# Kernel optimization log

Hardware: AMD Instinct MI355X
Metric: run time of the kernel (lower is better)

Reference implementation:

```python
import jax, jax.numpy as jnp
import numpy as np

B, S, D = 2, 4096, 768
H = 12
HD = D // H  # 64
INNER = 4 * D
EPS = 1e-5


def setup_inputs() -> dict:
    key = jax.random.key(0)
    ks = jax.random.split(key, 12)
    sd = 0.02
    # causal additive mask (GPT-2 style): 0 where allowed, -1e9 where masked
    causal = jnp.tril(jnp.ones((S, S), dtype=bool))
    attention_mask = jnp.where(causal, 0.0, -1e9).astype(jnp.float32)[None, None]
    return {
        "hidden_states": jax.random.normal(ks[0], (B, S, D), dtype=jnp.float32),
        "attention_mask": attention_mask,
        "ln1_g": jnp.ones((D,), jnp.float32),
        "ln1_b": jnp.zeros((D,), jnp.float32),
        "w_attn": jax.random.normal(ks[1], (D, 3 * D), jnp.float32) * sd,
        "b_attn": jnp.zeros((3 * D,), jnp.float32),
        "w_cproj": jax.random.normal(ks[2], (D, D), jnp.float32) * sd,
        "b_cproj": jnp.zeros((D,), jnp.float32),
        "ln2_g": jnp.ones((D,), jnp.float32),
        "ln2_b": jnp.zeros((D,), jnp.float32),
        "w_fc": jax.random.normal(ks[3], (D, INNER), jnp.float32) * sd,
        "b_fc": jnp.zeros((INNER,), jnp.float32),
        "w_fc_proj": jax.random.normal(ks[4], (INNER, D), jnp.float32) * sd,
        "b_fc_proj": jnp.zeros((D,), jnp.float32),
    }


def _layernorm(x, g, b):
    mu = jnp.mean(x, axis=-1, keepdims=True)
    var = jnp.mean(jnp.square(x - mu), axis=-1, keepdims=True)
    return (x - mu) * jax.lax.rsqrt(var + EPS) * g + b


def reference(hidden_states, attention_mask, ln1_g, ln1_b, w_attn, b_attn,
              w_cproj, b_cproj, ln2_g, ln2_b, w_fc, b_fc, w_fc_proj, b_fc_proj):
    residual = hidden_states
    x = _layernorm(hidden_states, ln1_g, ln1_b)
    # qkv projection
    qkv = x @ w_attn + b_attn                       # [B,S,3D]
    q, k, v = jnp.split(qkv, 3, axis=-1)
    q = q.reshape(B, S, H, HD).transpose(0, 2, 1, 3)  # [B,H,S,HD]
    k = k.reshape(B, S, H, HD).transpose(0, 2, 1, 3)
    v = v.reshape(B, S, H, HD).transpose(0, 2, 1, 3)
    scale = HD ** -0.5
    scores = jnp.einsum('bhqd,bhkd->bhqk', q, k) * scale + attention_mask
    attn = jax.nn.softmax(scores, axis=-1)
    ctx = jnp.einsum('bhqk,bhkd->bhqd', attn, v)    # [B,H,S,HD]
    ctx = ctx.transpose(0, 2, 1, 3).reshape(B, S, D)
    attn_out = ctx @ w_cproj + b_cproj
    h = attn_out + residual
    residual = h
    y = _layernorm(h, ln2_g, ln2_b)
    y = jax.nn.gelu(y @ w_fc + b_fc, approximate=False)  # nn.GELU default = exact
    y = y @ w_fc_proj + b_fc_proj
    return y + residual
```

## Files before the change

### kernel.cpp

```cpp
#include <hip/hip_runtime.h>
#include <hip/hip_bf16.h>


#define S_     4096
#define D_     768
#define H_     12
#define HD_    64
#define NB_    2
#define M_     (NB_*S_)
#define QKV_   (3*D_)
#define INNER_ 3072

typedef unsigned short u16;
typedef __attribute__((ext_vector_type(4))) float f32x4;
typedef __attribute__((ext_vector_type(8))) short s16x8;

__device__ __forceinline__ float bf2f(u16 h) {
    union { unsigned int u; float f; } c; c.u = ((unsigned int)h) << 16; return c.f;
}
__device__ __forceinline__ u16 f2bf(float f) {
    union { float f; unsigned int u; } c; c.f = f;
    return (u16)((c.u + 0x7fffu + ((c.u >> 16) & 1u)) >> 16);
}
__device__ __forceinline__ void storev(u16* p, float v) { *p = f2bf(v); }
__device__ __forceinline__ void storev(float* p, float v) { *p = v; }

__device__ __forceinline__ float fexp2(float x) {
#if __has_builtin(__builtin_amdgcn_exp2f)
    return __builtin_amdgcn_exp2f(x);
#else
    return __expf(x * 0.69314718056f);
#endif
}
__device__ __forceinline__ unsigned int packbf(float a, float b) {
    union { __hip_bfloat162 h; unsigned int u; } c;
    c.h = __float22bfloat162_rn(float2{a, b});
    return c.u;
}

__device__ __forceinline__ void gload_lds16(const u16* g, u16* l) {
    __builtin_amdgcn_global_load_lds((const __attribute__((address_space(1))) void*)g,
                                     (__attribute__((address_space(3))) void*)l, 16, 0, 0);
}

#define WAITVM(N) asm volatile("s_waitcnt vmcnt(" #N ")" ::: "memory")

template <typename IT, bool PERM>
__global__ __launch_bounds__(256) void transpose_kernel(const IT* __restrict__ in,
                                                        u16* __restrict__ out,
                                                        int ld_in, int ld_out) {
    __shared__ u16 tile[32][33];
    const int c0 = blockIdx.x * 32, r0 = blockIdx.y * 32;
    const int tx = threadIdx.x & 31, ty = threadIdx.x >> 5;
#pragma unroll
    for (int i = 0; i < 32; i += 8) {
        IT v = in[(size_t)(r0 + ty + i) * ld_in + c0 + tx];
        u16 bv;
        if constexpr (sizeof(IT) == 4) bv = f2bf((float)v); else bv = (u16)v;
        tile[ty + i][tx] = bv;
    }
    __syncthreads();
    int oc = r0 + tx;
    if constexpr (PERM) oc = (oc & ~63) | (((oc & 15) << 2) | ((oc >> 4) & 3));
#pragma unroll
    for (int i = 0; i < 32; i += 8)
        out[(size_t)(c0 + ty + i) * ld_out + oc] = tile[tx][ty + i];
}

__global__ __launch_bounds__(256) void ln_row(const float* __restrict__ x, const float* __restrict__ g,
                                              const float* __restrict__ bb, u16* __restrict__ y,
                                              unsigned int* ctr) {
    const int row = blockIdx.x;
    const int tid = threadIdx.x;
    if (ctr && row == 0 && tid == 0) *ctr = 0u;
    const float* xr = x + (size_t)row * D_;
    float v0 = xr[tid], v1 = xr[tid + 256], v2 = xr[tid + 512];
    float s = v0 + v1 + v2, s2 = v0 * v0 + v1 * v1 + v2 * v2;
#pragma unroll
    for (int d = 32; d >= 1; d >>= 1) { s += __shfl_xor(s, d, 64); s2 += __shfl_xor(s2, d, 64); }
    __shared__ float red[8];
    const int wave = tid >> 6, lane = tid & 63;
    if (lane == 0) { red[wave] = s; red[4 + wave] = s2; }
    __syncthreads();
    s = red[0] + red[1] + red[2] + red[3];
    s2 = red[4] + red[5] + red[6] + red[7];
    const float mu = s * (1.0f / D_);
    const float var = s2 * (1.0f / D_) - mu * mu;
    const float rstd = rsqrtf(var + 1e-5f);
    u16* yr = y + (size_t)row * D_;
    yr[tid]       = f2bf((v0 - mu) * rstd * g[tid]       + bb[tid]);
    yr[tid + 256] = f2bf((v1 - mu) * rstd * g[tid + 256] + bb[tid + 256]);
    yr[tid + 512] = f2bf((v2 - mu) * rstd * g[tid + 512] + bb[tid + 512]);
}

template <int EPI>
__global__ __launch_bounds__(512, 2) void gemm256(const u16* __restrict__ A, const u16* __restrict__ Bt,
                                                  const float* __restrict__ bias,
                                                  u16* __restrict__ C, int M, int N, int K, int nbx) {
    __shared__ u16 As[2][256 * 64];
    __shared__ u16 Bs[2][256 * 64];
    const int tid = threadIdx.x;
    const int wave = tid >> 6, lane = tid & 63;
    const int fr = lane & 15, quad = lane >> 4;
    const int wm = wave >> 2, wn = wave & 3;

    const int nwg = (int)gridDim.x;
    const int id = (int)blockIdx.x;
    const int swz = (id & 7) * (nwg >> 3) + (id >> 3);
    const int by = swz / nbx, bx = swz % nbx;
    const int m0 = by << 8, n0 = bx << 8;

    const int rsub = lane >> 3;
    const int schunk = ((lane & 7) ^ rsub) << 3;
    const u16* Ag = A + (size_t)(m0 + wave * 8 + rsub) * K + schunk;
    const u16* Bg = Bt + (size_t)(n0 + wave * 8 + rsub) * K + schunk;
    const int sdst = wave * 512;

    const f32x4 fz = {0.f, 0.f, 0.f, 0.f};
    f32x4 acc[8][4];
#pragma unroll
    for (int i = 0; i < 8; i++)
#pragma unroll
        for (int j = 0; j < 4; j++) acc[i][j] = fz;

    const int nt = K >> 6;

    auto STAGE_E = [&](int t, int b) {
        const int koff = t << 6;
#pragma unroll
        for (int g = 0; g < 4; g++)
            gload_lds16(Bg + (size_t)(g * 64) * K + koff, &Bs[b][g * 4096 + sdst]);
        gload_lds16(Ag + koff,                   &As[b][0 * 4096 + sdst]);
        gload_lds16(Ag + (size_t)128 * K + koff, &As[b][2 * 4096 + sdst]);
    };
    auto STAGE_L = [&](int t, int b) {
        const int koff = t << 6;
        gload_lds16(Ag + (size_t)64 * K + koff,  &As[b][1 * 4096 + sdst]);
        gload_lds16(Ag + (size_t)192 * K + koff, &As[b][3 * 4096 + sdst]);
    };

    STAGE_E(0, 0);
    STAGE_L(0, 0);
    WAITVM(2);

    for (int t = 0; t < nt; t++) {
        const int b = t & 1;
        __syncthreads();
        const u16* ab = As[b];
        const u16* bb = Bs[b];

        s16x8 bf[4][2], af[4][2];
#pragma unroll
        for (int j = 0; j < 4; j++)
#pragma unroll
            for (int kk = 0; kk < 2; kk++) {
                const int r = wn * 64 + j * 16 + fr;
                const int sl = ((kk * 4 + quad) ^ (r & 7)) << 3;
                bf[j][kk] = *(const s16x8*)(bb + r * 64 + sl);
            }
#pragma unroll
        for (int i = 0; i < 4; i++)
#pragma unroll
            for (int kk = 0; kk < 2; kk++) {
                const int r = wm * 128 + i * 16 + fr;
                const int sl = ((kk * 4 + quad) ^ (r & 7)) << 3;
                af[i][kk] = *(const s16x8*)(ab + r * 64 + sl);
            }
        if (t + 1 < nt) STAGE_E(t + 1, b ^ 1);
#pragma unroll
        for (int kk = 0; kk < 2; kk++)
#pragma unroll
            for (int i = 0; i < 4; i++)
#pragma unroll
                for (int j = 0; j < 4; j++)
                    acc[i][j] = __builtin_amdgcn_mfma_f32_16x16x32_bf16(af[i][kk], bf[j][kk], acc[i][j], 0, 0, 0);

        if (t + 1 < nt) { WAITVM(6); } else { WAITVM(0); }
        __syncthreads();

#pragma unroll
        for (int i = 0; i < 4; i++)
#pragma unroll
            for (int kk = 0; kk < 2; kk++) {
                const int r = wm * 128 + 64 + i * 16 + fr;
                const int sl = ((kk * 4 + quad) ^ (r & 7)) << 3;
                af[i][kk] = *(const s16x8*)(ab + r * 64 + sl);
            }
        if (t + 1 < nt) STAGE_L(t + 1, b ^ 1);
#pragma unroll
        for (int kk = 0; kk < 2; kk++)
#pragma unroll
            for (int i = 0; i < 4; i++)
#pragma unroll
                for (int j = 0; j < 4; j++)
                    acc[4 + i][j] = __builtin_amdgcn_mfma_f32_16x16x32_bf16(af[i][kk], bf[j][kk], acc[4 + i][j], 0, 0, 0);

        if (t + 1 < nt) WAITVM(2);
    }

    const int crow0 = m0 + wm * 128 + quad * 4;
    const int ccol0 = n0 + wn * 64 + fr;
#pragma unroll
    for (int j = 0; j < 4; j++) {
        const int col = ccol0 + j * 16;
        const float bv = bias[col];
#pragma unroll
        for (int i = 0; i < 8; i++) {
#pragma unroll
            for (int r = 0; r < 4; r++) {
                const int row = crow0 + i * 16 + r;
                float v = acc[i][j][r] + bv;
                if constexpr (EPI == 1) v = 0.5f * v * (1.0f + erff(v * 0.70710678118654752f));
                C[(size_t)row * N + col] = f2bf(v);
            }
        }
    }
}

template <int EPI, typename OT>
__global__ __launch_bounds__(256) void gemm_bt64(const u16* __restrict__ A, const u16* __restrict__ Bt,
                                                 const float* __restrict__ bias, const float* res,
                                                 OT* C, int M, int N, int K) {
    __shared__ u16 As[3][128 * 32];
    __shared__ u16 Bs[3][64 * 32];
    const int tid = threadIdx.x;
    const int wave = tid >> 6, lane = tid & 63;
    const int m0 = blockIdx.y << 7, n0 = blockIdx.x << 6;
    const int fr = lane & 15, quad = lane >> 4;

    const int srow = wave * 16 + (lane >> 2);
    const int scol = (lane & 3) * 8;
    const u16* ag0 = A + (size_t)(m0 + srow) * K + scol;
    const u16* ag1 = ag0 + (size_t)64 * K;
    const u16* bg0 = Bt + (size_t)(n0 + srow) * K + scol;

    auto STAGE = [&](int k0, int b) {
        gload_lds16(ag0 + k0, &As[b][wave * 512]);
        gload_lds16(ag1 + k0, &As[b][2048 + wave * 512]);
        gload_lds16(bg0 + k0, &Bs[b][wave * 512]);
    };

    const f32x4 fz = {0.f, 0.f, 0.f, 0.f};
    f32x4 acc[2][4];
#pragma unroll
    for (int i = 0; i < 2; i++)
#pragma unroll
        for (int j = 0; j < 4; j++) acc[i][j] = fz;

    const int a_off = (wave * 32 + fr) * 32 + quad * 8;
    const int b_off = fr * 32 + quad * 8;

    const int nsteps = K >> 5;
    STAGE(0, 0);
    if (nsteps > 1) { STAGE(32, 1); WAITVM(3); } else { WAITVM(0); }
    __syncthreads();

    for (int t = 0; t < nsteps; t++) {
        if (t + 2 < nsteps) STAGE((t + 2) << 5, (t + 2) % 3);
        const u16* a_rd = &As[t % 3][a_off];
        const u16* b_rd = &Bs[t % 3][b_off];
        s16x8 af[2], bfr[4];
#pragma unroll
        for (int u = 0; u < 2; u++) af[u] = *(const s16x8*)(a_rd + u * 16 * 32);
#pragma unroll
        for (int u = 0; u < 4; u++) bfr[u] = *(const s16x8*)(b_rd + u * 16 * 32);
#pragma unroll
        for (int mt = 0; mt < 2; mt++)
#pragma unroll
            for (int nt = 0; nt < 4; nt++)
                acc[mt][nt] = __builtin_amdgcn_mfma_f32_16x16x32_bf16(af[mt], bfr[nt], acc[mt][nt], 0, 0, 0);
        if (t + 2 < nsteps) { WAITVM(3); } else { WAITVM(0); }
        __syncthreads();
    }

    const int crow0 = m0 + wave * 32 + quad * 4;
    const int ccol0 = n0 + fr;
#pragma unroll
    for (int nt = 0; nt < 4; nt++) {
        const int col = ccol0 + nt * 16;
        const float bv = bias[col];
#pragma unroll
        for (int mt = 0; mt < 2; mt++) {
#pragma unroll
            for (int r = 0; r < 4; r++) {
                const int row = crow0 + mt * 16 + r;
                float v = acc[mt][nt][r] + bv;
                if constexpr (EPI == 1) v = 0.5f * v * (1.0f + erff(v * 0.70710678118654752f));
                if constexpr (EPI == 2) v += res[(size_t)row * N + col];
                storev(&C[(size_t)row * N + col], v);
            }
        }
    }
}

#define SCALE_  0.1803368801111f
#define PST_    72
#define NITEMS_ (32 * H_ * NB_)
#define NWORK_  512
__global__ __launch_bounds__(256, 2) void flash_attn(const u16* __restrict__ qkv, const u16* __restrict__ vt,
                                                     u16* __restrict__ ctx, unsigned int* __restrict__ ctr) {
    const int tid = threadIdx.x;
    const int wave = tid >> 6, lane = tid & 63;
    const int fr = lane & 15, quad = lane >> 4;

    __shared__ u16 Ks[2][64 * 64];
    __shared__ u16 Vs[2][64 * 64];
    __shared__ u16 Ps4[4][32 * PST_];
    __shared__ int item_sh;
    u16* Ps = Ps4[wave];

    const int rsub = lane >> 3;
    const int schunk = ((lane & 7) ^ rsub) << 3;
    u16* KlS0 = &Ks[0][(wave << 4) * 64];
    u16* VlS0 = &Vs[0][(wave << 4) * 64];

    const f32x4 fz = {0.f, 0.f, 0.f, 0.f};
    s16x8 ones;
#pragma unroll
    for (int j = 0; j < 8; j++) ones[j] = (short)0x3F80;

    for (;;) {
        if (tid == 0) item_sh = (int)atomicAdd(ctr, 1u);
        __syncthreads();
        const int item = item_sh;
        if (item >= NITEMS_) return;

        const int strip = 31 - item / (H_ * NB_);
        const int hb = item % (H_ * NB_);
        const int h = hb % H_, b = hb / H_;
        const int q0 = strip << 7;
        const int qwv = q0 + (wave << 5);

        const u16* Qg  = qkv + ((size_t)b * S_ + qwv) * QKV_ + h * HD_;
        const u16* Kg  = qkv + (size_t)b * S_ * QKV_ + D_ + h * HD_;
        const u16* Vtg = vt + ((size_t)b * D_ + h * HD_) * S_;
        const u16* KgS = Kg + (size_t)((wave << 4) + rsub) * QKV_ + schunk;
        const u16* VgS = Vtg + (size_t)((wave << 4) + rsub) * S_ + schunk;

        s16x8 qf[2][2];
#pragma unroll
        for (int mt = 0; mt < 2; mt++)
#pragma unroll
            for (int kk = 0; kk < 2; kk++)
                qf[mt][kk] = *(const s16x8*)(Qg + (size_t)(mt * 16 + fr) * QKV_ + kk * 32 + quad * 8);

        f32x4 o[2][4];
        f32x4 ls[2];
#pragma unroll
        for (int mt = 0; mt < 2; mt++) {
            ls[mt] = fz;
#pragma unroll
            for (int nt = 0; nt < 4; nt++) o[mt][nt] = fz;
        }

        const int ntw = (strip << 1) + 2;

        gload_lds16(KgS, KlS0);
        gload_lds16(KgS + (size_t)8 * QKV_, KlS0 + 512);
        gload_lds16(VgS, VlS0);
        gload_lds16(VgS + (size_t)8 * S_, VlS0 + 512);
        asm volatile("s_waitcnt vmcnt(0)" ::: "memory");
        __syncthreads();

        int cur = 0;
        for (int t = 0; t < ntw; t++) {
            const int k0 = t << 6;

            if (t + 1 < ntw) {
                const int nb = cur ^ 1;
                const u16* kg = KgS + (size_t)((t + 1) << 6) * QKV_;
                const u16* vg = VgS + ((t + 1) << 6);
                u16* kl = KlS0 + nb * (64 * 64);
                u16* vl = VlS0 + nb * (64 * 64);
                gload_lds16(kg, kl);
                gload_lds16(kg + (size_t)8 * QKV_, kl + 512);
                gload_lds16(vg, vl);
                gload_lds16(vg + (size_t)8 * S_, vl + 512);
            }

            if (k0 <= qwv + 31) {
                const u16* kb = Ks[cur];
                const u16* vb = Vs[cur];

                s16x8 kc[2][4];
#pragma unroll
                for (int kk = 0; kk < 2; kk++)
#pragma unroll
                    for (int nt = 0; nt < 4; nt++) {
                        const int row = nt * 16 + fr;
                        const int sl = ((kk * 4 + quad) ^ (fr & 7)) << 3;
                        kc[kk][nt] = *(const s16x8*)(kb + row * 64 + sl);
                    }

                f32x4 sc[2][4];
#pragma unroll
                for (int mt = 0; mt < 2; mt++)
#pragma unroll
                    for (int nt = 0; nt < 4; nt++) sc[mt][nt] = fz;
#pragma unroll
                for (int kk = 0; kk < 2; kk++)
#pragma unroll
                    for (int mt = 0; mt < 2; mt++)
#pragma unroll
                        for (int nt = 0; nt < 4; nt++)
                            sc[mt][nt] = __builtin_amdgcn_mfma_f32_16x16x32_bf16(qf[mt][kk], kc[kk][nt], sc[mt][nt], 0, 0, 0);

                const bool fast = (k0 + 63 <= qwv);
#pragma unroll
                for (int mt = 0; mt < 2; mt++) {
#pragma unroll
                    for (int r = 0; r < 4; r++) {
                        float s0 = sc[mt][0][r] * SCALE_;
                        float s1 = sc[mt][1][r] * SCALE_;
                        float s2 = sc[mt][2][r] * SCALE_;
                        float s3 = sc[mt][3][r] * SCALE_;
                        if (!fast) {
                            const int lim = (qwv + mt * 16 + quad * 4 + r) - k0;
                            if (fr      > lim) s0 = -1e30f;
                            if (fr + 16 > lim) s1 = -1e30f;
                            if (fr + 32 > lim) s2 = -1e30f;
                            if (fr + 48 > lim) s3 = -1e30f;
                        }
                        s0 = fexp2(s0); s1 = fexp2(s1); s2 = fexp2(s2); s3 = fexp2(s3);
                        const int prow = mt * 16 + quad * 4 + r;
                        *(uint2*)(Ps + prow * PST_ + fr * 4) = make_uint2(packbf(s0, s1), packbf(s2, s3));
                    }
                }

                s16x8 vf[2][4];
#pragma unroll
                for (int kk = 0; kk < 2; kk++)
#pragma unroll
                    for (int nt = 0; nt < 4; nt++) {
                        const int row = nt * 16 + fr;
                        const int sl = ((kk * 4 + quad) ^ (fr & 7)) << 3;
                        vf[kk][nt] = *(const s16x8*)(vb + row * 64 + sl);
                    }

                s16x8 pf[2][2];
#pragma unroll
                for (int mt = 0; mt < 2; mt++)
#pragma unroll
                    for (int kk = 0; kk < 2; kk++)
                        pf[mt][kk] = *(const s16x8*)(Ps + (mt * 16 + fr) * PST_ + kk * 32 + quad * 8);

#pragma unroll
                for (int mt = 0; mt < 2; mt++) {
                    ls[mt] = __builtin_amdgcn_mfma_f32_16x16x32_bf16(pf[mt][0], ones, ls[mt], 0, 0, 0);
                    ls[mt] = __builtin_amdgcn_mfma_f32_16x16x32_bf16(pf[mt][1], ones, ls[mt], 0, 0, 0);
                }
#pragma unroll
                for (int kk = 0; kk < 2; kk++)
#pragma unroll
                    for (int mt = 0; mt < 2; mt++)
#pragma unroll
                        for (int nt = 0; nt < 4; nt++)
                            o[mt][nt] = __builtin_amdgcn_mfma_f32_16x16x32_bf16(pf[mt][kk], vf[kk][nt], o[mt][nt], 0, 0, 0);
            }

            asm volatile("s_waitcnt vmcnt(0)" ::: "memory");
            __syncthreads();
            cur ^= 1;
        }

#pragma unroll
        for (int mt = 0; mt < 2; mt++) {
#pragma unroll
            for (int r = 0; r < 4; r++) {
                const int grow = qwv + mt * 16 + quad * 4 + r;
                const float inv = 1.0f / ls[mt][r];
                u16* crow = ctx + ((size_t)b * S_ + grow) * D_ + h * HD_ + fr;
#pragma unroll
                for (int nt = 0; nt < 4; nt++)
                    crow[nt * 16] = f2bf(o[mt][nt][r] * inv);
            }
        }
    }
}

extern "C" void kernel_launch(void* const* d_in, const int* in_sizes, int n_in,
                              void* d_out, int out_size, void* d_ws, size_t ws_size,
                              hipStream_t stream) {
    const float* hid    = (const float*)d_in[0];
    const float* ln1g   = (const float*)d_in[2];
    const float* ln1b   = (const float*)d_in[3];
    const float* w_attn = (const float*)d_in[4];
    const float* b_attn = (const float*)d_in[5];
    const float* w_cp   = (const float*)d_in[6];
    const float* b_cp   = (const float*)d_in[7];
    const float* ln2g   = (const float*)d_in[8];
    const float* ln2b   = (const float*)d_in[9];
    const float* w_fc   = (const float*)d_in[10];
    const float* b_fc   = (const float*)d_in[11];
    const float* w_fp   = (const float*)d_in[12];
    const float* b_fp   = (const float*)d_in[13];
    float* dout = (float*)d_out;

    unsigned int* ctr = (unsigned int*)d_out;

    u16* ws = (u16*)d_ws;
    u16* wTa  = ws; ws += (size_t)QKV_ * D_;
    u16* wTc  = ws; ws += (size_t)D_ * D_;
    u16* wTf  = ws; ws += (size_t)INNER_ * D_;
    u16* wTp  = ws; ws += (size_t)D_ * INNER_;
    u16* xln  = ws; ws += (size_t)M_ * D_;
    u16* qkvb = ws; ws += (size_t)M_ * QKV_;
    u16* vtb  = ws; ws += (size_t)NB_ * D_ * S_;
    u16* ctxb = xln;
    u16* yln  = xln;
    u16* act  = qkvb;

    dim3 blk(256);
    transpose_kernel<float, false><<<dim3(QKV_ / 32, D_ / 32), blk, 0, stream>>>(w_attn, wTa, QKV_, D_);
    transpose_kernel<float, false><<<dim3(D_ / 32, D_ / 32), blk, 0, stream>>>(w_cp, wTc, D_, D_);
    transpose_kernel<float, false><<<dim3(INNER_ / 32, D_ / 32), blk, 0, stream>>>(w_fc, wTf, INNER_, D_);
    transpose_kernel<float, false><<<dim3(D_ / 32, INNER_ / 32), blk, 0, stream>>>(w_fp, wTp, D_, INNER_);

    ln_row<<<M_, blk, 0, stream>>>(hid, ln1g, ln1b, xln, ctr);
    gemm256<0><<<dim3(288), dim3(512), 0, stream>>>(xln, wTa, b_attn, qkvb, M_, QKV_, D_, 9);

    transpose_kernel<u16, true><<<dim3(D_ / 32, S_ / 32), blk, 0, stream>>>(qkvb + 2 * D_, vtb, QKV_, S_);
    transpose_kernel<u16, true><<<dim3(D_ / 32, S_ / 32), blk, 0, stream>>>(qkvb + (size_t)S_ * QKV_ + 2 * D_,
                                                                            vtb + (size_t)D_ * S_, QKV_, S_);
    flash_attn<<<dim3(NWORK_), blk, 0, stream>>>(qkvb, vtb, ctxb, ctr);

    gemm_bt64<2, float><<<dim3(D_ / 64, M_ / 128), blk, 0, stream>>>(ctxb, wTc, b_cp, hid, dout, M_, D_, D_);
    ln_row<<<M_, blk, 0, stream>>>(dout, ln2g, ln2b, yln, nullptr);
    gemm256<1><<<dim3(384), dim3(512), 0, stream>>>(yln, wTf, b_fc, act, M_, INNER_, D_, 12);
    gemm_bt64<2, float><<<dim3(D_ / 64, M_ / 128), blk, 0, stream>>>(act, wTp, b_fp, dout, dout, M_, D_, INNER_);
}
```

Baseline: 583.8 us.

## Restructure gemm256 into k-half staged ping-pong pipeline with priority hints

Splits each 64-wide K tile of the 256x256 GEMM into two 32-wide halves with separate LDS buffers and a new XOR swizzle. Each half is loaded piecewise (A then B) interleaved with MFMA phases, separated by raw s_barrier calls and s_setprio hints. The goal is finer-grained overlap of global-to-LDS copies with MFMA work and fewer LDS bank conflicts. It also drops the min-2-blocks launch bound and adds an XCD-aware block-index swizzle to gemm_bt64 for L2 locality. The cost is many more barriers per K step and the risk of lower occupancy.

```diff
diff --git a/kernel.cpp b/kernel.cpp
--- a/kernel.cpp
+++ b/kernel.cpp
@@ -44,6 +44,7 @@
 }
 
 #define WAITVM(N) asm volatile("s_waitcnt vmcnt(" #N ")" ::: "memory")
+#define MEMFENCE  asm volatile("" ::: "memory")
 
 template <typename IT, bool PERM>
 __global__ __launch_bounds__(256) void transpose_kernel(const IT* __restrict__ in,
@@ -94,27 +95,27 @@
 }
 
 template <int EPI>
-__global__ __launch_bounds__(512, 2) void gemm256(const u16* __restrict__ A, const u16* __restrict__ Bt,
-                                                  const float* __restrict__ bias,
-                                                  u16* __restrict__ C, int M, int N, int K, int nbx) {
-    __shared__ u16 As[2][256 * 64];
-    __shared__ u16 Bs[2][256 * 64];
+__global__ __launch_bounds__(512) void gemm256(const u16* __restrict__ A, const u16* __restrict__ Bt,
+                                               const float* __restrict__ bias,
+                                               u16* __restrict__ C, int M, int N, int K, int nbx) {
+    __shared__ u16 As[2][2][256 * 32];
+    __shared__ u16 Bs[2][2][256 * 32];
     const int tid = threadIdx.x;
     const int wave = tid >> 6, lane = tid & 63;
     const int fr = lane & 15, quad = lane >> 4;
     const int wm = wave >> 2, wn = wave & 3;
 
     const int nwg = (int)gridDim.x;
-    const int id = (int)blockIdx.x;
-    const int swz = (id & 7) * (nwg >> 3) + (id >> 3);
-    const int by = swz / nbx, bx = swz % nbx;
+    int id = (int)blockIdx.x;
+    id = (id & 7) * (nwg >> 3) + (id >> 3);
+    const int by = id / nbx, bx = id % nbx;
     const int m0 = by << 8, n0 = bx << 8;
 
-    const int rsub = lane >> 3;
-    const int schunk = ((lane & 7) ^ rsub) << 3;
-    const u16* Ag = A + (size_t)(m0 + wave * 8 + rsub) * K + schunk;
-    const u16* Bg = Bt + (size_t)(n0 + wave * 8 + rsub) * K + schunk;
-    const int sdst = wave * 512;
+    const int rsub = lane >> 2;
+    const int gch = ((lane & 3) ^ (rsub & 3)) << 3;
+    const u16* AgS = A + (size_t)(m0 + wave * 16 + rsub) * K + gch;
+    const u16* BgS = Bt + (size_t)(n0 + wave * 16 + rsub) * K + gch;
+    const int ldst = (wave * 16) * 32;
 
     const f32x4 fz = {0.f, 0.f, 0.f, 0.f};
     f32x4 acc[8][4];
@@ -125,77 +126,96 @@
 
     const int nt = K >> 6;
 
-    auto STAGE_E = [&](int t, int b) {
-        const int koff = t << 6;
-#pragma unroll
-        for (int g = 0; g < 4; g++)
-            gload_lds16(Bg + (size_t)(g * 64) * K + koff, &Bs[b][g * 4096 + sdst]);
-        gload_lds16(Ag + koff,                   &As[b][0 * 4096 + sdst]);
-        gload_lds16(Ag + (size_t)128 * K + koff, &As[b][2 * 4096 + sdst]);
+    auto STAGE_A = [&](int t, int kh) {
+        const u16* src = AgS + (size_t)t * 64 + kh * 32;
+        u16* dst = &As[t & 1][kh][ldst];
+        gload_lds16(src, dst);
+        gload_lds16(src + (size_t)128 * K, dst + 128 * 32);
     };
-    auto STAGE_L = [&](int t, int b) {
-        const int koff = t << 6;
-        gload_lds16(Ag + (size_t)64 * K + koff,  &As[b][1 * 4096 + sdst]);
-        gload_lds16(Ag + (size_t)192 * K + koff, &As[b][3 * 4096 + sdst]);
+    auto STAGE_B = [&](int t, int kh) {
+        const u16* src = BgS + (size_t)t * 64 + kh * 32;
+        u16* dst = &Bs[t & 1][kh][ldst];
+        gload_lds16(src, dst);
+        gload_lds16(src + (size_t)128 * K, dst + 128 * 32);
     };
 
-    STAGE_E(0, 0);
-    STAGE_L(0, 0);
-    WAITVM(2);
+    const int fsl = fr & 3;
+    auto LDA = [&](const u16* base, int a) -> s16x8 {
+        const int row = wm * 128 + a * 16 + fr;
+        return *(const s16x8*)(base + row * 32 + ((quad ^ fsl) << 3));
+    };
+    auto LDB = [&](const u16* base, int j) -> s16x8 {
+        const int row = wn * 64 + j * 16 + fr;
+        return *(const s16x8*)(base + row * 32 + ((quad ^ fsl) << 3));
+    };
+
+    STAGE_A(0, 0); STAGE_B(0, 0); STAGE_A(0, 1); STAGE_B(0, 1);
+    WAITVM(4);
+    MEMFENCE; __builtin_amdgcn_s_barrier(); MEMFENCE;
 
     for (int t = 0; t < nt; t++) {
-        const int b = t & 1;
-        __syncthreads();
-        const u16* ab = As[b];
-        const u16* bb = Bs[b];
-
-        s16x8 bf[4][2], af[4][2];
-#pragma unroll
-        for (int j = 0; j < 4; j++)
-#pragma unroll
-            for (int kk = 0; kk < 2; kk++) {
-                const int r = wn * 64 + j * 16 + fr;
-                const int sl = ((kk * 4 + quad) ^ (r & 7)) << 3;
-                bf[j][kk] = *(const s16x8*)(bb + r * 64 + sl);
-            }
+        const int buf = t & 1;
+        const u16* a0 = As[buf][0]; const u16* a1 = As[buf][1];
+        const u16* b0 = Bs[buf][0]; const u16* b1 = Bs[buf][1];
+        s16x8 af[4], bfv[4];
+
+#pragma unroll
+        for (int j = 0; j < 4; j++) bfv[j] = LDB(b0, j);
+#pragma unroll
+        for (int i = 0; i < 4; i++) af[i] = LDA(a0, i);
+        if (t + 1 < nt) STAGE_A(t + 1, 0);
+        MEMFENCE; __builtin_amdgcn_s_barrier(); MEMFENCE;
+        __builtin_amdgcn_s_setprio(1);
 #pragma unroll
         for (int i = 0; i < 4; i++)
 #pragma unroll
-            for (int kk = 0; kk < 2; kk++) {
-                const int r = wm * 128 + i * 16 + fr;
-                const int sl = ((kk * 4 + quad) ^ (r & 7)) << 3;
-                af[i][kk] = *(const s16x8*)(ab + r * 64 + sl);
-            }
-        if (t + 1 < nt) STAGE_E(t + 1, b ^ 1);
-#pragma unroll
-        for (int kk = 0; kk < 2; kk++)
-#pragma unroll
-            for (int i = 0; i < 4; i++)
-#pragma unroll
-                for (int j = 0; j < 4; j++)
-                    acc[i][j] = __builtin_amdgcn_mfma_f32_16x16x32_bf16(af[i][kk], bf[j][kk], acc[i][j], 0, 0, 0);
-
-        if (t + 1 < nt) { WAITVM(6); } else { WAITVM(0); }
-        __syncthreads();
-
+            for (int j = 0; j < 4; j++)
+                acc[i][j] = __builtin_amdgcn_mfma_f32_16x16x32_bf16(af[i], bfv[j], acc[i][j], 0, 0, 0);
+        __builtin_amdgcn_s_setprio(0);
+        MEMFENCE; __builtin_amdgcn_s_barrier(); MEMFENCE;
+
+#pragma unroll
+        for (int i = 0; i < 4; i++) af[i] = LDA(a0, 4 + i);
+        if (t + 1 < nt) STAGE_B(t + 1, 0);
+        MEMFENCE; __builtin_amdgcn_s_barrier(); MEMFENCE;
+        __builtin_amdgcn_s_setprio(1);
 #pragma unroll
         for (int i = 0; i < 4; i++)
 #pragma unroll
-            for (int kk = 0; kk < 2; kk++) {
-                const int r = wm * 128 + 64 + i * 16 + fr;
-                const int sl = ((kk * 4 + quad) ^ (r & 7)) << 3;
-                af[i][kk] = *(const s16x8*)(ab + r * 64 + sl);
-            }
-        if (t + 1 < nt) STAGE_L(t + 1, b ^ 1);
-#pragma unroll
-        for (int kk = 0; kk < 2; kk++)
-#pragma unroll
-            for (int i = 0; i < 4; i++)
-#pragma unroll
-                for (int j = 0; j < 4; j++)
-                    acc[4 + i][j] = __builtin_amdgcn_mfma_f32_16x16x32_bf16(af[i][kk], bf[j][kk], acc[4 + i][j], 0, 0, 0);
-
-        if (t + 1 < nt) WAITVM(2);
+            for (int j = 0; j < 4; j++)
+                acc[4 + i][j] = __builtin_amdgcn_mfma_f32_16x16x32_bf16(af[i], bfv[j], acc[4 + i][j], 0, 0, 0);
+        __builtin_amdgcn_s_setprio(0);
+        if (t + 1 < nt) { WAITVM(4); } else { WAITVM(0); }
+        MEMFENCE; __builtin_amdgcn_s_barrier(); MEMFENCE;
+
+#pragma unroll
+        for (int j = 0; j < 4; j++) bfv[j] = LDB(b1, j);
+#pragma unroll
+        for (int i = 0; i < 4; i++) af[i] = LDA(a1, i);
+        if (t + 1 < nt) STAGE_A(t + 1, 1);
+        MEMFENCE; __builtin_amdgcn_s_barrier(); MEMFENCE;
+        __builtin_amdgcn_s_setprio(1);
+#pragma unroll
+        for (int i = 0; i < 4; i++)
+#pragma unroll
+            for (int j = 0; j < 4; j++)
+                acc[i][j] = __builtin_amdgcn_mfma_f32_16x16x32_bf16(af[i], bfv[j], acc[i][j], 0, 0, 0);
+        __builtin_amdgcn_s_setprio(0);
+        MEMFENCE; __builtin_amdgcn_s_barrier(); MEMFENCE;
+
+#pragma unroll
+        for (int i = 0; i < 4; i++) af[i] = LDA(a1, 4 + i);
+        if (t + 1 < nt) STAGE_B(t + 1, 1);
+        MEMFENCE; __builtin_amdgcn_s_barrier(); MEMFENCE;
+        __builtin_amdgcn_s_setprio(1);
+#pragma unroll
+        for (int i = 0; i < 4; i++)
+#pragma unroll
+            for (int j = 0; j < 4; j++)
+                acc[4 + i][j] = __builtin_amdgcn_mfma_f32_16x16x32_bf16(af[i], bfv[j], acc[4 + i][j], 0, 0, 0);
+        __builtin_amdgcn_s_setprio(0);
+        WAITVM(4);
+        MEMFENCE; __builtin_amdgcn_s_barrier(); MEMFENCE;
     }
 
     const int crow0 = m0 + wm * 128 + quad * 4;
@@ -205,11 +225,11 @@
         const int col = ccol0 + j * 16;
         const float bv = bias[col];
 #pragma unroll
-        for (int i = 0; i < 8; i++) {
+        for (int a = 0; a < 8; a++) {
 #pragma unroll
             for (int r = 0; r < 4; r++) {
-                const int row = crow0 + i * 16 + r;
-                float v = acc[i][j][r] + bv;
+                const int row = crow0 + a * 16 + r;
+                float v = acc[a][j][r] + bv;
                 if constexpr (EPI == 1) v = 0.5f * v * (1.0f + erff(v * 0.70710678118654752f));
                 C[(size_t)row * N + col] = f2bf(v);
             }
@@ -225,8 +245,13 @@
     __shared__ u16 Bs[3][64 * 32];
     const int tid = threadIdx.x;
     const int wave = tid >> 6, lane = tid & 63;
-    const int m0 = blockIdx.y << 7, n0 = blockIdx.x << 6;
     const int fr = lane & 15, quad = lane >> 4;
+
+    const int nwg = (int)(gridDim.x * gridDim.y);
+    int id = (int)(blockIdx.y * gridDim.x + blockIdx.x);
+    id = (id & 7) * (nwg >> 3) + (id >> 3);
+    const int by = id / (int)gridDim.x, bx = id % (int)gridDim.x;
+    const int m0 = by << 7, n0 = bx << 6;
 
     const int srow = wave * 16 + (lane >> 2);
     const int scol = (lane & 3) * 8;
```

New measurement: 549.3 us. 5.9% less time.
